# Kernel optimization log

Measured on AMD Instinct MI355X. Metric: run time of the kernel, lower is better.

## Reference

```python
import jax, jax.numpy as jnp
import numpy as np

B, N, DIN, DH, H_MLP, L, C = 64, 1024, 64, 128, 128, 3, 4


def setup_inputs() -> dict:
    key = jax.random.key(0)
    ks = jax.random.split(key, 12)
    s = 0.05  # weight scale for numerical stability
    return {
        "x": jax.random.normal(ks[0], (B, N, DIN), jnp.float32),
        "U": jax.random.normal(ks[1], (3, N, N), jnp.float32) / np.sqrt(N),
        "w1_0": jax.random.normal(ks[2], (3, DIN, H_MLP), jnp.float32) * s,
        "b1_0": jnp.zeros((3, H_MLP), jnp.float32),
        "w2_0": jax.random.normal(ks[3], (3, H_MLP, DH), jnp.float32) * s,
        "b2_0": jnp.zeros((3, DH), jnp.float32),
        "w1_r": jax.random.normal(ks[4], (L - 1, 3, DH, H_MLP), jnp.float32) * s,
        "b1_r": jnp.zeros((L - 1, 3, H_MLP), jnp.float32),
        "w2_r": jax.random.normal(ks[5], (L - 1, 3, H_MLP, DH), jnp.float32) * s,
        "b2_r": jnp.zeros((L - 1, 3, DH), jnp.float32),
        "bw": jnp.ones((L, 3), jnp.float32),  # weight1/2/3 init to 1.0 per layer
        "Wc1": jax.random.normal(ks[6], (DH, 128), jnp.float32) * s,
        "bc1": jnp.zeros((128,), jnp.float32),
        "alpha": jnp.full((128,), 0.25, jnp.float32),  # PReLU init
        "Wc2": jax.random.normal(ks[7], (128, C), jnp.float32) * s,
        "bc2": jnp.zeros((C,), jnp.float32),
    }


def _gcn_multi(h, U, w1, b1, w2, b2, w3):
    """One GraphConv_multi layer: 3 spectral branches, softmax-weighted sum.
    h: [B,N,D_in], U: [3,N,N], w1:[3,Din,H], w2:[3,H,Dout], w3:[3]."""
    # agg = U^T @ h per branch (U is shared across batch; no repeat needed)
    agg = jnp.einsum('kji,bjd->kbid', U, h)                     # [3,B,N,Din]
    m = jax.nn.relu(jnp.einsum('kbid,kdh->kbih', agg, w1) + b1[:, None, None, :])
    m = jnp.einsum('kbih,kho->kbio', m, w2) + b2[:, None, None, :]  # [3,B,N,Dout]
    out = jnp.einsum('kij,kbjd->kbid', U, m)                    # U @ mlp_out
    ws = jax.nn.softmax(w3)                                     # branch mix
    return jnp.einsum('k,kbid->bid', ws, out)


def reference(x, U, w1_0, b1_0, w2_0, b2_0, w1_r, b1_r, w2_r, b2_r,
              bw, Wc1, bc1, alpha, Wc2, bc2):
    h = jax.nn.relu(_gcn_multi(x, U, w1_0, b1_0, w2_0, b2_0, bw[0]))
    for l in range(w1_r.shape[0]):  # remaining num_layers-1 GCN layers
        h = jax.nn.relu(_gcn_multi(h, U, w1_r[l], b1_r[l], w2_r[l], b2_r[l], bw[l + 1]))
    pooled = jnp.mean(h, axis=1)                                # 'mean' graph pooling
    z = pooled @ Wc1 + bc1
    z = jnp.where(z > 0, z, alpha * z)                          # PReLU(128); dropout = eval no-op
    return z @ Wc2 + bc2                                        # [B, C]
```

## Files before the change

kernel.cpp:

```cpp
#include <hip/hip_runtime.h>


typedef unsigned short u16;
typedef short bf16x8 __attribute__((ext_vector_type(8)));
typedef float f32x4 __attribute__((ext_vector_type(4)));
typedef u16 u16x4 __attribute__((ext_vector_type(4)));

__device__ __forceinline__ u16 f2bf(float x){
  unsigned u = __builtin_bit_cast(unsigned, x);
  u += 0x7fffu + ((u >> 16) & 1u);
  return (u16)(u >> 16);
}
__device__ __forceinline__ float bf2f(u16 h){
  return __builtin_bit_cast(float, ((unsigned)h) << 16);
}
__device__ __forceinline__ void gload16(const u16* g, u16* l){
  __builtin_amdgcn_global_load_lds(
      (const __attribute__((address_space(1))) unsigned int*)(g),
      (__attribute__((address_space(3))) unsigned int*)(l), 16, 0, 0);
}


__global__ void prep_weights(const float* __restrict__ w1_0, const float* __restrict__ w2_0,
                             const float* __restrict__ w1_r, const float* __restrict__ w2_r,
                             const float* __restrict__ bw,
                             u16* __restrict__ W1T0, u16* __restrict__ W2T0,
                             u16* __restrict__ W1Tr, u16* __restrict__ W2Tr,
                             float* __restrict__ wsb){
  int id = blockIdx.x*256 + threadIdx.x;
  if (id < 3){
    float a0=bw[id*3+0], a1=bw[id*3+1], a2=bw[id*3+2];
    float m = fmaxf(a0,fmaxf(a1,a2));
    float e0=expf(a0-m), e1=expf(a1-m), e2=expf(a2-m);
    float s = e0+e1+e2;
    wsb[id*3+0]=e0/s; wsb[id*3+1]=e1/s; wsb[id*3+2]=e2/s;
  }
  if (id < 24576){
    int k=id/8192, rem=id%8192, h=rem/64, d=rem%64;
    W1T0[id] = f2bf(w1_0[(k*64+d)*128 + h]);
  } else if (id < 73728){
    int t=id-24576, k=t/16384, rem=t%16384, o=rem/128, h=rem%128;
    W2T0[t] = f2bf(w2_0[(k*128+h)*128 + o]);
  } else if (id < 172032){
    int t=id-73728, lk=t/16384, rem=t%16384, h=rem/128, d=rem%128;
    W1Tr[t] = f2bf(w1_r[lk*16384 + d*128 + h]);
  } else if (id < 270336){
    int t=id-172032, lk=t/16384, rem=t%16384, o=rem/128, h=rem%128;
    W2Tr[t] = f2bf(w2_r[lk*16384 + h*128 + o]);
  }
}

__global__ void prep_U(const float* __restrict__ U, u16* __restrict__ UTcat,
                       u16* __restrict__ Ucat){
  __shared__ float t[32][33];
  int k = blockIdx.z, i0 = blockIdx.x*32, j0 = blockIdx.y*32;
  size_t kb = (size_t)k << 20;
  #pragma unroll
  for (int rr=0; rr<4; rr++){
    int r = threadIdx.y*4+rr, c = threadIdx.x;
    float v = U[kb + (size_t)(j0+r)*1024 + i0+c];
    t[r][c] = v;
    Ucat[(size_t)(j0+r)*3072 + k*1024 + i0+c] = f2bf(v);
  }
  __syncthreads();
  #pragma unroll
  for (int rr=0; rr<4; rr++){
    int r = threadIdx.y*4+rr, c = threadIdx.x;
    UTcat[kb + (size_t)(i0+r)*1024 + j0+c] = f2bf(t[c][r]);
  }
}

__global__ void prep_x(const float* __restrict__ x, u16* __restrict__ H){
  __shared__ float t[32][33];
  int b = blockIdx.z, d0 = blockIdx.x*32, j0 = blockIdx.y*32;
  #pragma unroll
  for (int rr=0;rr<4;rr++){
    int r=threadIdx.y*4+rr, c=threadIdx.x;
    t[r][c] = x[((size_t)b*1024 + j0+r)*64 + d0+c];
  }
  __syncthreads();
  #pragma unroll
  for (int rr=0;rr<4;rr++){
    int r=threadIdx.y*4+rr, c=threadIdx.x;
    H[(size_t)(b*64 + d0+r)*1024 + j0+c] = f2bf(t[c][r]);
  }
}

template<bool RELU, int REORD>
__global__ __launch_bounds__(512)
void gemm_big(const u16* __restrict__ A, const u16* __restrict__ B,
              u16* __restrict__ C, int Nc, int K, long aZ, int cRowZ)
{
  __shared__ __align__(16) u16 ldsA[3*16384];
  __shared__ __align__(16) u16 ldsB[3*8192];
  const int tid = threadIdx.x;
  const int z = blockIdx.z;
  const u16* Ab = A + (size_t)z*aZ;
  const int gx = gridDim.x;
  const int nwg = gx*gridDim.y;
  int flat = blockIdx.y*gx + blockIdx.x;
  if ((nwg & 7) == 0) flat = (flat & 7)*(nwg >> 3) + (flat >> 3);
  const int bm = (flat/gx)*256, bn = (flat%gx)*128;
  const int wave = tid>>6, lane = tid&63;
  const int wm = (wave&3)*64, wn = (wave>>2)*64;
  const int rl = lane&15, ksb = lane>>4;
  const int xr = (rl&7)<<3;
  const int srow = tid>>3;
  const int scol = ((tid&7)*8) ^ ((srow&7)<<3);
  const int NT = K>>6;

  f32x4 acc[4][4];
  #pragma unroll
  for (int mi=0;mi<4;mi++)
    #pragma unroll
    for (int ni=0;ni<4;ni++){ f32x4 zv={0.f,0.f,0.f,0.f}; acc[mi][ni]=zv; }

  auto stage = [&](int t){
    const int sa = (t%3)*16384, sb = (t%3)*8192;
    const int k0 = t<<6;
    #pragma unroll
    for (int c=0;c<4;c++){
      const int row = c*64 + srow;
      gload16(Ab + (size_t)(bm+row)*K + k0 + scol, &ldsA[sa + c*4096 + tid*8]);
    }
    #pragma unroll
    for (int c=0;c<2;c++){
      const int row = c*64 + srow;
      gload16(B + (size_t)(bn+row)*K + k0 + scol, &ldsB[sb + c*4096 + tid*8]);
    }
  };

  stage(0); stage(1);
  asm volatile("s_waitcnt vmcnt(6)" ::: "memory");
  __builtin_amdgcn_s_barrier();
  __builtin_amdgcn_sched_barrier(0);

  for (int t=0; t<NT; t++){
    const int sa = (t%3)*16384, sb = (t%3)*8192;
    bf16x8 af[4][2], bfr[4][2];
    #pragma unroll
    for (int mi=0;mi<4;mi++){
      const int row = wm + mi*16 + rl;
      #pragma unroll
      for (int kk=0;kk<2;kk++)
        af[mi][kk] = *(const bf16x8*)&ldsA[sa + row*64 + ((kk*32 + ksb*8) ^ xr)];
    }
    #pragma unroll
    for (int ni=0;ni<4;ni++){
      const int row = wn + ni*16 + rl;
      #pragma unroll
      for (int kk=0;kk<2;kk++)
        bfr[ni][kk] = *(const bf16x8*)&ldsB[sb + row*64 + ((kk*32 + ksb*8) ^ xr)];
    }
    if (t+2 < NT) stage(t+2);
    __builtin_amdgcn_s_setprio(1);
    #pragma unroll
    for (int kk=0;kk<2;kk++)
      #pragma unroll
      for (int ni=0;ni<4;ni++)
        #pragma unroll
        for (int mi=0;mi<4;mi++)
          acc[mi][ni] = __builtin_amdgcn_mfma_f32_16x16x32_bf16(af[mi][kk], bfr[ni][kk], acc[mi][ni], 0,0,0);
    __builtin_amdgcn_s_setprio(0);
    if (t+2 < NT)      asm volatile("s_waitcnt vmcnt(6)" ::: "memory");
    else if (t+1 < NT) asm volatile("s_waitcnt vmcnt(0)" ::: "memory");
    __builtin_amdgcn_s_barrier();
    __builtin_amdgcn_sched_barrier(0);
  }

  #pragma unroll
  for (int ni=0;ni<4;ni++){
    const int col = bn + wn + ni*16 + rl;
    #pragma unroll
    for (int mi=0;mi<4;mi++){
      const int row0 = bm + wm + mi*16 + ksb*4;
      #pragma unroll
      for (int r=0;r<4;r++){
        float v = acc[mi][ni][r];
        if (RELU) v = fmaxf(v, 0.f);
        if constexpr (REORD){
          const int Din = 1 << REORD;
          const int bb = col >> REORD, d = col & (Din-1);
          C[((size_t)((z<<6) + bb)*1024 + row0 + r)*Din + d] = f2bf(v);
        } else {
          C[(size_t)(z*cRowZ + row0 + r)*Nc + col] = f2bf(v);
        }
      }
    }
  }
}

template<bool RELU>
__global__ __launch_bounds__(256)
void gemm_bf16(const u16* __restrict__ A, const u16* __restrict__ B,
               u16* __restrict__ C, const float* __restrict__ bias,
               int Nc, int K, long aZ, long bZ, int cRowZ, int biasZ)
{
  __shared__ __align__(16) u16 lA[4096];
  __shared__ __align__(16) u16 lB[4096];
  const int tid = threadIdx.x;
  const int z = blockIdx.z;
  const u16* Ab = A + (size_t)z * aZ;
  const u16* Bb = B + (size_t)z * bZ;
  const int bm = blockIdx.y * 128, bn = blockIdx.x * 128;
  const int wave = tid >> 6, lane = tid & 63;
  const int wm = (wave >> 1) * 64, wn = (wave & 1) * 64;
  const int rl = lane & 15, ksb = lane >> 4;
  const int ar0 = tid >> 2, ak0 = (tid & 3) * 8;

  f32x4 acc[4][4];
  #pragma unroll
  for (int mi=0;mi<4;mi++)
    #pragma unroll
    for (int ni=0;ni<4;ni++){ f32x4 zv={0.f,0.f,0.f,0.f}; acc[mi][ni]=zv; }

  for (int k0=0; k0<K; k0+=32){
    __syncthreads();
    gload16(Ab + (size_t)(bm+ar0   )*K + k0+ak0, &lA[tid*8]);
    gload16(Ab + (size_t)(bm+ar0+64)*K + k0+ak0, &lA[2048 + tid*8]);
    gload16(Bb + (size_t)(bn+ar0   )*K + k0+ak0, &lB[tid*8]);
    gload16(Bb + (size_t)(bn+ar0+64)*K + k0+ak0, &lB[2048 + tid*8]);
    __syncthreads();
    bf16x8 af[4], bfv[4];
    #pragma unroll
    for (int i=0;i<4;i++){
      af[i]  = *(const bf16x8*)&lA[(wm+i*16+rl)*32 + ksb*8];
      bfv[i] = *(const bf16x8*)&lB[(wn+i*16+rl)*32 + ksb*8];
    }
    #pragma unroll
    for (int ni=0;ni<4;ni++)
      #pragma unroll
      for (int mi=0;mi<4;mi++)
        acc[mi][ni] = __builtin_amdgcn_mfma_f32_16x16x32_bf16(af[mi], bfv[ni], acc[mi][ni], 0,0,0);
  }

  #pragma unroll
  for (int ni=0;ni<4;ni++){
    const int col = bn + wn + ni*16 + rl;
    const float bv = bias ? bias[z*biasZ + col] : 0.0f;
    #pragma unroll
    for (int mi=0;mi<4;mi++){
      const int row0 = z*cRowZ + bm + wm + mi*16 + ksb*4;
      #pragma unroll
      for (int r=0;r<4;r++){
        float v = acc[mi][ni][r] + bv;
        if (RELU) v = fmaxf(v, 0.f);
        C[(size_t)(row0+r)*Nc + col] = f2bf(v);
      }
    }
  }
}

__global__ __launch_bounds__(256)
void gemm_mlp2t(const u16* __restrict__ W2T, const u16* __restrict__ M1,
                u16* __restrict__ M2T, const float* __restrict__ b2,
                const float* __restrict__ wsl)
{
  __shared__ __align__(16) u16 lA[4096];
  __shared__ __align__(16) u16 lB[4096];
  const int tid = threadIdx.x;
  const int z = blockIdx.z, k = z>>6, b = z&63;
  const u16* Ab = W2T + k*16384;
  const u16* Bb = M1  + (size_t)z*131072;
  const int bn = blockIdx.x*128;
  const int wave = tid>>6, lane = tid&63;
  const int wm = (wave>>1)*64, wn = (wave&1)*64;
  const int rl = lane&15, ksb = lane>>4;
  const int ar0 = tid>>2, ak0 = (tid&3)*8;
  const float ws = wsl[k];

  f32x4 acc[4][4];
  #pragma unroll
  for (int mi=0;mi<4;mi++)
    #pragma unroll
    for (int ni=0;ni<4;ni++){ f32x4 zv={0.f,0.f,0.f,0.f}; acc[mi][ni]=zv; }

  for (int k0=0; k0<128; k0+=32){
    __syncthreads();
    gload16(Ab + (size_t)(ar0   )*128 + k0+ak0, &lA[tid*8]);
    gload16(Ab + (size_t)(ar0+64)*128 + k0+ak0, &lA[2048 + tid*8]);
    gload16(Bb + (size_t)(bn+ar0   )*128 + k0+ak0, &lB[tid*8]);
    gload16(Bb + (size_t)(bn+ar0+64)*128 + k0+ak0, &lB[2048 + tid*8]);
    __syncthreads();
    bf16x8 af[4], bfv[4];
    #pragma unroll
    for (int i=0;i<4;i++){
      af[i]  = *(const bf16x8*)&lA[(wm+i*16+rl)*32 + ksb*8];
      bfv[i] = *(const bf16x8*)&lB[(wn+i*16+rl)*32 + ksb*8];
    }
    #pragma unroll
    for (int ni=0;ni<4;ni++)
      #pragma unroll
      for (int mi=0;mi<4;mi++)
        acc[mi][ni] = __builtin_amdgcn_mfma_f32_16x16x32_bf16(af[mi], bfv[ni], acc[mi][ni], 0,0,0);
  }

  float bvv[4][4];
  #pragma unroll
  for (int mi=0;mi<4;mi++)
    #pragma unroll
    for (int r=0;r<4;r++)
      bvv[mi][r] = b2[k*128 + wm + mi*16 + ksb*4 + r];

  #pragma unroll
  for (int ni=0;ni<4;ni++){
    const int j = bn + wn + ni*16 + rl;
    #pragma unroll
    for (int mi=0;mi<4;mi++){
      const int o0 = wm + mi*16 + ksb*4;
      #pragma unroll
      for (int r=0;r<4;r++){
        float v = (acc[mi][ni][r] + bvv[mi][r]) * ws;
        M2T[(size_t)(b*128 + o0 + r)*3072 + k*1024 + j] = f2bf(v);
      }
    }
  }
}

__global__ void pool_kernel(const u16* __restrict__ H, float* __restrict__ pooled){
  const int row = blockIdx.x, t = threadIdx.x;
  u16x4 v = *(const u16x4*)(H + (size_t)row*1024 + t*4);
  float s = bf2f(v.x)+bf2f(v.y)+bf2f(v.z)+bf2f(v.w);
  for (int o2=32;o2>0;o2>>=1) s += __shfl_down(s,o2);
  __shared__ float red[4];
  if ((t&63)==0) red[t>>6]=s;
  __syncthreads();
  if (t==0) pooled[row] = (red[0]+red[1]+red[2]+red[3])*(1.f/1024.f);
}

__global__ void head_kernel(const float* __restrict__ pooled, const float* __restrict__ Wc1,
                            const float* __restrict__ bc1, const float* __restrict__ alpha,
                            const float* __restrict__ Wc2, const float* __restrict__ bc2,
                            float* __restrict__ out){
  const int b = blockIdx.x, h = threadIdx.x;
  __shared__ float p[128], zz[128];
  p[h] = pooled[b*128+h];
  __syncthreads();
  float acc = bc1[h];
  for (int d=0; d<128; d++) acc = fmaf(p[d], Wc1[d*128+h], acc);
  zz[h] = acc>0.f ? acc : alpha[h]*acc;
  __syncthreads();
  if (h<4){
    float a = bc2[h];
    for (int q=0;q<128;q++) a = fmaf(zz[q], Wc2[q*4+h], a);
    out[b*4+h]=a;
  }
}

extern "C" void kernel_launch(void* const* d_in, const int* in_sizes, int n_in,
                              void* d_out, int out_size, void* d_ws, size_t ws_size,
                              hipStream_t stream)
{
  const float* x     = (const float*)d_in[0];
  const float* U     = (const float*)d_in[1];
  const float* w1_0  = (const float*)d_in[2];
  const float* b1_0  = (const float*)d_in[3];
  const float* w2_0  = (const float*)d_in[4];
  const float* b2_0  = (const float*)d_in[5];
  const float* w1_r  = (const float*)d_in[6];
  const float* b1_r  = (const float*)d_in[7];
  const float* w2_r  = (const float*)d_in[8];
  const float* b2_r  = (const float*)d_in[9];
  const float* bw    = (const float*)d_in[10];
  const float* Wc1   = (const float*)d_in[11];
  const float* bc1   = (const float*)d_in[12];
  const float* alpha = (const float*)d_in[13];
  const float* Wc2   = (const float*)d_in[14];
  const float* bc2   = (const float*)d_in[15];
  float* out = (float*)d_out;

  char* wsp = (char*)d_ws;
  size_t off = 0;
  auto alloc = [&](size_t bytes) -> void* {
    void* p = wsp + off;
    off = (off + bytes + 255) & ~(size_t)255;
    return p;
  };
  u16* UTcat = (u16*)alloc(6291456);
  u16* Ucat  = (u16*)alloc(6291456);
  u16* W1T0  = (u16*)alloc(49152);
  u16* W2T0  = (u16*)alloc(98304);
  u16* W1Tr  = (u16*)alloc(196608);
  u16* W2Tr  = (u16*)alloc(196608);
  float* wsb = (float*)alloc(256);
  u16* HT    = (u16*)alloc(16777216);
  u16* AGG   = (u16*)alloc(50331648);
  u16* M1    = (u16*)alloc(50331648);
  float* pooled = (float*)alloc(32768);
  if (off > ws_size) return;

  prep_weights<<<1056, 256, 0, stream>>>(w1_0,w2_0,w1_r,w2_r,bw,
      W1T0,W2T0,W1Tr,W2Tr,wsb);
  prep_U<<<dim3(32,32,3), dim3(32,8), 0, stream>>>(U, UTcat, Ucat);
  prep_x<<<dim3(2,32,64), dim3(32,8), 0, stream>>>(x, HT);

  for (int l=0; l<3; l++){
    const int Din = l ? 128 : 64;
    const u16* w1t = l ? W1Tr + (size_t)(l-1)*3*16384 : W1T0;
    const long w1Z = l ? 16384 : 8192;
    const u16* w2t = l ? W2Tr + (size_t)(l-1)*3*16384 : W2T0;
    const float* b1 = l ? b1_r + (l-1)*384 : b1_0;
    const float* b2 = l ? b2_r + (l-1)*384 : b2_0;

    if (l == 0)
      gemm_big<false,6><<<dim3(32, 4, 3), 512, 0, stream>>>(
          UTcat, HT, AGG, 4096, 1024, 1048576L, 0);
    else
      gemm_big<false,7><<<dim3(64, 4, 3), 512, 0, stream>>>(
          UTcat, HT, AGG, 8192, 1024, 1048576L, 0);
    gemm_bf16<true><<<dim3(1, 512, 3), 256, 0, stream>>>(
        AGG, w1t, M1, b1, 128, Din, (long)65536*Din, w1Z, 65536, 128);
    gemm_mlp2t<<<dim3(8, 1, 192), 256, 0, stream>>>(w2t, M1, AGG, b2, wsb + l*3);
    gemm_big<true,0><<<dim3(8, 32, 1), 512, 0, stream>>>(
        AGG, Ucat, HT, 1024, 3072, 0L, 0);
  }
  pool_kernel<<<8192, 256, 0, stream>>>(HT, pooled);
  head_kernel<<<64, 128, 0, stream>>>(pooled, Wc1, bc1, alpha, Wc2, bc2, out);
}
```

Measured before the change: 476.4 us.

## Fuse the two MLP GEMMs into one kernel and split gemm_big k-step staging

The two per-branch MLP matmuls (first layer with bias+ReLU, second with bias and branch weight) become one kernel that keeps the hidden activations in LDS. This removes the M1 round trip through global memory and one launch per layer. The main aggregation GEMM's 64-wide k-step is also split into two 32-wide halves, with A and B staging interleaved between them and extra barriers added, to overlap loads with MFMA more finely. The fused kernel uses a larger LDS footprint per block, which may lower occupancy, and the extra barriers add synchronisation cost.

```diff
diff --git a/kernel.cpp b/kernel.cpp
--- a/kernel.cpp
+++ b/kernel.cpp
@@ -115,14 +115,18 @@
     #pragma unroll
     for (int ni=0;ni<4;ni++){ f32x4 zv={0.f,0.f,0.f,0.f}; acc[mi][ni]=zv; }
 
-  auto stage = [&](int t){
-    const int sa = (t%3)*16384, sb = (t%3)*8192;
+  auto stageA = [&](int t){
+    const int sa = (t%3)*16384;
     const int k0 = t<<6;
     #pragma unroll
     for (int c=0;c<4;c++){
       const int row = c*64 + srow;
       gload16(Ab + (size_t)(bm+row)*K + k0 + scol, &ldsA[sa + c*4096 + tid*8]);
     }
+  };
+  auto stageB = [&](int t){
+    const int sb = (t%3)*8192;
+    const int k0 = t<<6;
     #pragma unroll
     for (int c=0;c<2;c++){
       const int row = c*64 + srow;
@@ -130,37 +134,48 @@
     }
   };
 
-  stage(0); stage(1);
+  stageA(0); stageB(0); stageA(1); stageB(1);
   asm volatile("s_waitcnt vmcnt(6)" ::: "memory");
   __builtin_amdgcn_s_barrier();
   __builtin_amdgcn_sched_barrier(0);
 
   for (int t=0; t<NT; t++){
     const int sa = (t%3)*16384, sb = (t%3)*8192;
-    bf16x8 af[4][2], bfr[4][2];
-    #pragma unroll
-    for (int mi=0;mi<4;mi++){
-      const int row = wm + mi*16 + rl;
-      #pragma unroll
-      for (int kk=0;kk<2;kk++)
-        af[mi][kk] = *(const bf16x8*)&ldsA[sa + row*64 + ((kk*32 + ksb*8) ^ xr)];
-    }
-    #pragma unroll
-    for (int ni=0;ni<4;ni++){
-      const int row = wn + ni*16 + rl;
-      #pragma unroll
-      for (int kk=0;kk<2;kk++)
-        bfr[ni][kk] = *(const bf16x8*)&ldsB[sb + row*64 + ((kk*32 + ksb*8) ^ xr)];
-    }
-    if (t+2 < NT) stage(t+2);
+    bf16x8 a0[4], b0[4];
+    #pragma unroll
+    for (int mi=0;mi<4;mi++)
+      a0[mi] = *(const bf16x8*)&ldsA[sa + (wm+mi*16+rl)*64 + ((ksb*8) ^ xr)];
+    #pragma unroll
+    for (int ni=0;ni<4;ni++)
+      b0[ni] = *(const bf16x8*)&ldsB[sb + (wn+ni*16+rl)*64 + ((ksb*8) ^ xr)];
+    if (t+2 < NT) stageA(t+2);
+    __builtin_amdgcn_s_barrier();
+    __builtin_amdgcn_sched_barrier(0);
     __builtin_amdgcn_s_setprio(1);
     #pragma unroll
-    for (int kk=0;kk<2;kk++)
-      #pragma unroll
-      for (int ni=0;ni<4;ni++)
-        #pragma unroll
-        for (int mi=0;mi<4;mi++)
-          acc[mi][ni] = __builtin_amdgcn_mfma_f32_16x16x32_bf16(af[mi][kk], bfr[ni][kk], acc[mi][ni], 0,0,0);
+    for (int ni=0;ni<4;ni++)
+      #pragma unroll
+      for (int mi=0;mi<4;mi++)
+        acc[mi][ni] = __builtin_amdgcn_mfma_f32_16x16x32_bf16(a0[mi], b0[ni], acc[mi][ni], 0,0,0);
+    __builtin_amdgcn_s_setprio(0);
+    __builtin_amdgcn_s_barrier();
+    __builtin_amdgcn_sched_barrier(0);
+    bf16x8 a1[4], b1v[4];
+    #pragma unroll
+    for (int mi=0;mi<4;mi++)
+      a1[mi] = *(const bf16x8*)&ldsA[sa + (wm+mi*16+rl)*64 + ((32 + ksb*8) ^ xr)];
+    #pragma unroll
+    for (int ni=0;ni<4;ni++)
+      b1v[ni] = *(const bf16x8*)&ldsB[sb + (wn+ni*16+rl)*64 + ((32 + ksb*8) ^ xr)];
+    if (t+2 < NT) stageB(t+2);
+    __builtin_amdgcn_s_barrier();
+    __builtin_amdgcn_sched_barrier(0);
+    __builtin_amdgcn_s_setprio(1);
+    #pragma unroll
+    for (int ni=0;ni<4;ni++)
+      #pragma unroll
+      for (int mi=0;mi<4;mi++)
+        acc[mi][ni] = __builtin_amdgcn_mfma_f32_16x16x32_bf16(a1[mi], b1v[ni], acc[mi][ni], 0,0,0);
     __builtin_amdgcn_s_setprio(0);
     if (t+2 < NT)      asm volatile("s_waitcnt vmcnt(6)" ::: "memory");
     else if (t+1 < NT) asm volatile("s_waitcnt vmcnt(0)" ::: "memory");
@@ -190,128 +205,118 @@
   }
 }
 
-template<bool RELU>
+template<int DIN>
 __global__ __launch_bounds__(256)
-void gemm_bf16(const u16* __restrict__ A, const u16* __restrict__ B,
-               u16* __restrict__ C, const float* __restrict__ bias,
-               int Nc, int K, long aZ, long bZ, int cRowZ, int biasZ)
+void fused_mlp(const u16* __restrict__ AGG, const u16* __restrict__ W1T,
+               const u16* __restrict__ W2T, const float* __restrict__ b1g,
+               const float* __restrict__ b2g, const float* __restrict__ wsl,
+               u16* __restrict__ M2T)
 {
-  __shared__ __align__(16) u16 lA[4096];
-  __shared__ __align__(16) u16 lB[4096];
+  constexpr int JW1 = 128*DIN;
+  __shared__ __align__(16) u16 lds[2*JW1 + 16384];
   const int tid = threadIdx.x;
-  const int z = blockIdx.z;
-  const u16* Ab = A + (size_t)z * aZ;
-  const u16* Bb = B + (size_t)z * bZ;
-  const int bm = blockIdx.y * 128, bn = blockIdx.x * 128;
-  const int wave = tid >> 6, lane = tid & 63;
-  const int wm = (wave >> 1) * 64, wn = (wave & 1) * 64;
-  const int rl = lane & 15, ksb = lane >> 4;
-  const int ar0 = tid >> 2, ak0 = (tid & 3) * 8;
-
-  f32x4 acc[4][4];
-  #pragma unroll
-  for (int mi=0;mi<4;mi++)
-    #pragma unroll
-    for (int ni=0;ni<4;ni++){ f32x4 zv={0.f,0.f,0.f,0.f}; acc[mi][ni]=zv; }
-
-  for (int k0=0; k0<K; k0+=32){
-    __syncthreads();
-    gload16(Ab + (size_t)(bm+ar0   )*K + k0+ak0, &lA[tid*8]);
-    gload16(Ab + (size_t)(bm+ar0+64)*K + k0+ak0, &lA[2048 + tid*8]);
-    gload16(Bb + (size_t)(bn+ar0   )*K + k0+ak0, &lB[tid*8]);
-    gload16(Bb + (size_t)(bn+ar0+64)*K + k0+ak0, &lB[2048 + tid*8]);
-    __syncthreads();
-    bf16x8 af[4], bfv[4];
-    #pragma unroll
-    for (int i=0;i<4;i++){
-      af[i]  = *(const bf16x8*)&lA[(wm+i*16+rl)*32 + ksb*8];
-      bfv[i] = *(const bf16x8*)&lB[(wn+i*16+rl)*32 + ksb*8];
-    }
-    #pragma unroll
-    for (int ni=0;ni<4;ni++)
-      #pragma unroll
-      for (int mi=0;mi<4;mi++)
-        acc[mi][ni] = __builtin_amdgcn_mfma_f32_16x16x32_bf16(af[mi], bfv[ni], acc[mi][ni], 0,0,0);
-  }
-
-  #pragma unroll
-  for (int ni=0;ni<4;ni++){
-    const int col = bn + wn + ni*16 + rl;
-    const float bv = bias ? bias[z*biasZ + col] : 0.0f;
-    #pragma unroll
-    for (int mi=0;mi<4;mi++){
-      const int row0 = z*cRowZ + bm + wm + mi*16 + ksb*4;
-      #pragma unroll
-      for (int r=0;r<4;r++){
-        float v = acc[mi][ni][r] + bv;
-        if (RELU) v = fmaxf(v, 0.f);
-        C[(size_t)(row0+r)*Nc + col] = f2bf(v);
-      }
-    }
-  }
-}
-
-__global__ __launch_bounds__(256)
-void gemm_mlp2t(const u16* __restrict__ W2T, const u16* __restrict__ M1,
-                u16* __restrict__ M2T, const float* __restrict__ b2,
-                const float* __restrict__ wsl)
-{
-  __shared__ __align__(16) u16 lA[4096];
-  __shared__ __align__(16) u16 lB[4096];
-  const int tid = threadIdx.x;
-  const int z = blockIdx.z, k = z>>6, b = z&63;
-  const u16* Ab = W2T + k*16384;
-  const u16* Bb = M1  + (size_t)z*131072;
-  const int bn = blockIdx.x*128;
+  const int jt = blockIdx.x, z = blockIdx.z, k = z>>6, b = z&63;
+  const u16* Ag  = AGG + ((size_t)z*1024 + jt*128)*DIN;
+  const u16* W1k = W1T + k*JW1;
+  const u16* W2k = W2T + k*16384;
   const int wave = tid>>6, lane = tid&63;
   const int wm = (wave>>1)*64, wn = (wave&1)*64;
   const int rl = lane&15, ksb = lane>>4;
-  const int ar0 = tid>>2, ak0 = (tid&3)*8;
+  const int xr = (rl&7)<<3;
+
+  constexpr int CJ = JW1/2048;
+  #pragma unroll
+  for (int c=0;c<CJ;c++){
+    const int e = c*2048 + tid*8, row = e/DIN, col = e%DIN;
+    gload16(Ag + (size_t)row*DIN + (col ^ ((row&7)<<3)), &lds[e]);
+  }
+  #pragma unroll
+  for (int c=0;c<CJ;c++){
+    const int e = c*2048 + tid*8, row = e/DIN, col = e%DIN;
+    gload16(W1k + (size_t)row*DIN + (col ^ ((row&7)<<3)), &lds[JW1 + e]);
+  }
+  #pragma unroll
+  for (int c=0;c<8;c++){
+    const int e = c*2048 + tid*8, row = e>>7, col = e&127;
+    gload16(W2k + (size_t)row*128 + (col ^ ((row&7)<<3)), &lds[2*JW1 + e]);
+  }
+  asm volatile("s_waitcnt vmcnt(8)" ::: "memory");
+  __builtin_amdgcn_s_barrier();
+  __builtin_amdgcn_sched_barrier(0);
+
+  f32x4 acc[4][4];
+  #pragma unroll
+  for (int mi=0;mi<4;mi++)
+    #pragma unroll
+    for (int ni=0;ni<4;ni++){ f32x4 zv={0.f,0.f,0.f,0.f}; acc[mi][ni]=zv; }
+  #pragma unroll
+  for (int k0=0; k0<DIN; k0+=32){
+    bf16x8 aj[4], wh[4];
+    #pragma unroll
+    for (int mi=0;mi<4;mi++)
+      aj[mi] = *(const bf16x8*)&lds[(wm+mi*16+rl)*DIN + ((k0+ksb*8) ^ xr)];
+    #pragma unroll
+    for (int ni=0;ni<4;ni++)
+      wh[ni] = *(const bf16x8*)&lds[JW1 + (wn+ni*16+rl)*DIN + ((k0+ksb*8) ^ xr)];
+    #pragma unroll
+    for (int ni=0;ni<4;ni++)
+      #pragma unroll
+      for (int mi=0;mi<4;mi++)
+        acc[mi][ni] = __builtin_amdgcn_mfma_f32_16x16x32_bf16(aj[mi], wh[ni], acc[mi][ni], 0,0,0);
+  }
+  __syncthreads();
+
+  float bh[4];
+  #pragma unroll
+  for (int ni=0;ni<4;ni++) bh[ni] = b1g[k*128 + wn + ni*16 + rl];
+  #pragma unroll
+  for (int ni=0;ni<4;ni++){
+    const int h = wn + ni*16 + rl;
+    #pragma unroll
+    for (int mi=0;mi<4;mi++){
+      #pragma unroll
+      for (int r=0;r<4;r++){
+        const int j = wm + mi*16 + ksb*4 + r;
+        const float v = fmaxf(acc[mi][ni][r] + bh[ni], 0.f);
+        lds[j*128 + (h ^ ((j&7)<<3))] = f2bf(v);
+      }
+    }
+  }
+  __syncthreads();
+
+  f32x4 acc2[4][4];
+  #pragma unroll
+  for (int mi=0;mi<4;mi++)
+    #pragma unroll
+    for (int ni=0;ni<4;ni++){ f32x4 zv={0.f,0.f,0.f,0.f}; acc2[mi][ni]=zv; }
+  #pragma unroll
+  for (int k0=0; k0<128; k0+=32){
+    bf16x8 ao[4], mj[4];
+    #pragma unroll
+    for (int mi=0;mi<4;mi++)
+      ao[mi] = *(const bf16x8*)&lds[2*JW1 + (wm+mi*16+rl)*128 + ((k0+ksb*8) ^ xr)];
+    #pragma unroll
+    for (int ni=0;ni<4;ni++)
+      mj[ni] = *(const bf16x8*)&lds[(wn+ni*16+rl)*128 + ((k0+ksb*8) ^ xr)];
+    #pragma unroll
+    for (int ni=0;ni<4;ni++)
+      #pragma unroll
+      for (int mi=0;mi<4;mi++)
+        acc2[mi][ni] = __builtin_amdgcn_mfma_f32_16x16x32_bf16(ao[mi], mj[ni], acc2[mi][ni], 0,0,0);
+  }
+
   const float ws = wsl[k];
-
-  f32x4 acc[4][4];
-  #pragma unroll
-  for (int mi=0;mi<4;mi++)
-    #pragma unroll
-    for (int ni=0;ni<4;ni++){ f32x4 zv={0.f,0.f,0.f,0.f}; acc[mi][ni]=zv; }
-
-  for (int k0=0; k0<128; k0+=32){
-    __syncthreads();
-    gload16(Ab + (size_t)(ar0   )*128 + k0+ak0, &lA[tid*8]);
-    gload16(Ab + (size_t)(ar0+64)*128 + k0+ak0, &lA[2048 + tid*8]);
-    gload16(Bb + (size_t)(bn+ar0   )*128 + k0+ak0, &lB[tid*8]);
-    gload16(Bb + (size_t)(bn+ar0+64)*128 + k0+ak0, &lB[2048 + tid*8]);
-    __syncthreads();
-    bf16x8 af[4], bfv[4];
-    #pragma unroll
-    for (int i=0;i<4;i++){
-      af[i]  = *(const bf16x8*)&lA[(wm+i*16+rl)*32 + ksb*8];
-      bfv[i] = *(const bf16x8*)&lB[(wn+i*16+rl)*32 + ksb*8];
-    }
-    #pragma unroll
-    for (int ni=0;ni<4;ni++)
-      #pragma unroll
-      for (int mi=0;mi<4;mi++)
-        acc[mi][ni] = __builtin_amdgcn_mfma_f32_16x16x32_bf16(af[mi], bfv[ni], acc[mi][ni], 0,0,0);
-  }
-
-  float bvv[4][4];
-  #pragma unroll
-  for (int mi=0;mi<4;mi++)
-    #pragma unroll
-    for (int r=0;r<4;r++)
-      bvv[mi][r] = b2[k*128 + wm + mi*16 + ksb*4 + r];
-
-  #pragma unroll
-  for (int ni=0;ni<4;ni++){
-    const int j = bn + wn + ni*16 + rl;
-    #pragma unroll
-    for (int mi=0;mi<4;mi++){
-      const int o0 = wm + mi*16 + ksb*4;
-      #pragma unroll
-      for (int r=0;r<4;r++){
-        float v = (acc[mi][ni][r] + bvv[mi][r]) * ws;
-        M2T[(size_t)(b*128 + o0 + r)*3072 + k*1024 + j] = f2bf(v);
+  #pragma unroll
+  for (int mi=0;mi<4;mi++){
+    #pragma unroll
+    for (int r=0;r<4;r++){
+      const int o = wm + mi*16 + ksb*4 + r;
+      const float bo = b2g[k*128 + o];
+      #pragma unroll
+      for (int ni=0;ni<4;ni++){
+        const int j = wn + ni*16 + rl;
+        const float v = (acc2[mi][ni][r] + bo) * ws;
+        M2T[(size_t)(b*128 + o)*3072 + k*1024 + jt*128 + j] = f2bf(v);
       }
     }
   }
@@ -385,7 +390,7 @@
   float* wsb = (float*)alloc(256);
   u16* HT    = (u16*)alloc(16777216);
   u16* AGG   = (u16*)alloc(50331648);
-  u16* M1    = (u16*)alloc(50331648);
+  u16* M2T   = (u16*)alloc(50331648);
   float* pooled = (float*)alloc(32768);
   if (off > ws_size) return;
 
@@ -395,9 +400,7 @@
   prep_x<<<dim3(2,32,64), dim3(32,8), 0, stream>>>(x, HT);
 
   for (int l=0; l<3; l++){
-    const int Din = l ? 128 : 64;
     const u16* w1t = l ? W1Tr + (size_t)(l-1)*3*16384 : W1T0;
-    const long w1Z = l ? 16384 : 8192;
     const u16* w2t = l ? W2Tr + (size_t)(l-1)*3*16384 : W2T0;
     const float* b1 = l ? b1_r + (l-1)*384 : b1_0;
     const float* b2 = l ? b2_r + (l-1)*384 : b2_0;
@@ -408,11 +411,14 @@
     else
       gemm_big<false,7><<<dim3(64, 4, 3), 512, 0, stream>>>(
           UTcat, HT, AGG, 8192, 1024, 1048576L, 0);
-    gemm_bf16<true><<<dim3(1, 512, 3), 256, 0, stream>>>(
-        AGG, w1t, M1, b1, 128, Din, (long)65536*Din, w1Z, 65536, 128);
-    gemm_mlp2t<<<dim3(8, 1, 192), 256, 0, stream>>>(w2t, M1, AGG, b2, wsb + l*3);
+    if (l == 0)
+      fused_mlp<64><<<dim3(8, 1, 192), 256, 0, stream>>>(
+          AGG, w1t, w2t, b1, b2, wsb + l*3, M2T);
+    else
+      fused_mlp<128><<<dim3(8, 1, 192), 256, 0, stream>>>(
+          AGG, w1t, w2t, b1, b2, wsb + l*3, M2T);
     gemm_big<true,0><<<dim3(8, 32, 1), 512, 0, stream>>>(
-        AGG, Ucat, HT, 1024, 3072, 0L, 0);
+        M2T, Ucat, HT, 1024, 3072, 0L, 0);
   }
   pool_kernel<<<8192, 256, 0, stream>>>(HT, pooled);
   head_kernel<<<64, 128, 0, stream>>>(pooled, Wc1, bc1, alpha, Wc2, bc2, out);
```

After: 477.5 us. About the same (+0.2%).
